# Kernel optimization log

Hardware: AMD Instinct MI355X
Metric: run time of the kernel (lower is better)

Reference implementation:

```python
import jax, jax.numpy as jnp
import numpy as np
from jax import lax

T, B, IN = 50, 1024, 405
H, NMEM, DMEM, R, NWAY = 200, 128, 40, 4, 5
GAMMA = 0.99


def setup_inputs() -> dict:
    key = jax.random.key(0)
    ks = jax.random.split(key, 11)
    s = lambda *sh: 0.05
    return {
        "x": jax.random.normal(ks[0], (T, B, IN), jnp.float32),
        "W_ih": jax.random.normal(ks[1], (4 * H, IN), jnp.float32) * 0.05,
        "W_hh": jax.random.normal(ks[2], (4 * H, H), jnp.float32) * 0.05,
        "b_ih": jax.random.normal(ks[3], (4 * H,), jnp.float32) * 0.05,
        "b_hh": jax.random.normal(ks[4], (4 * H,), jnp.float32) * 0.05,
        "Wk": jax.random.normal(ks[5], (R * DMEM, H), jnp.float32) * 0.05,
        "bk": jax.random.normal(ks[6], (R * DMEM,), jnp.float32) * 0.05,
        "Ws": jax.random.normal(ks[7], (R, H), jnp.float32) * 0.05,
        "bs": jax.random.normal(ks[8], (R,), jnp.float32) * 0.05,
        "Wo": jax.random.normal(ks[9], (NWAY, H + R * DMEM), jnp.float32) * 0.05,
        "bo": jax.random.normal(ks[10], (NWAY,), jnp.float32) * 0.05,
    }


def _ntm_forward(x, W_ih, W_hh, b_ih, b_hh, Wk, bk, Ws, bs, Wo, bo):
    sg = lax.stop_gradient
    batch_idx = jnp.arange(B)

    def step(carry, x_t):
        h, c, M, wr, wu, wlu = carry
        # LSTM cell (torch nn.LSTMCell gate order: i, f, g, o)
        gates = x_t @ W_ih.T + b_ih + h @ W_hh.T + b_hh
        i, f, g, o = jnp.split(gates, 4, axis=-1)
        c = jax.nn.sigmoid(f) * c + jax.nn.sigmoid(i) * jnp.tanh(g)
        h = jax.nn.sigmoid(o) * jnp.tanh(c)
        # zero out least-used memory row (data-level op in torch)
        idx = jnp.argmin(wu, axis=1)
        M = M.at[batch_idx, idx].set(0.0)
        # keys and interpolation gate
        k = jnp.tanh(h @ Wk.T + bk).reshape(B, R, DMEM)
        sigma = jax.nn.sigmoid(jnp.tanh(h @ Ws.T + bs)).reshape(B, R, 1)
        # write weights and memory write
        ww = sigma * wr + (1.0 - sigma) * wlu[:, None, :]  # [B,R,NMEM]
        M = M + jnp.einsum("brm,brd->bmd", ww, k)
        # cosine-similarity read addressing
        nk = jnp.linalg.norm(k, axis=2)   # [B,R]
        nM = jnp.linalg.norm(M, axis=2)   # [B,NMEM]
        K = jnp.einsum("brd,bmd->brm", k, M) / (nk[:, :, None] * nM[:, None, :])
        wr_new = jax.nn.softmax(K, axis=-1)  # softmax over memory slots
        r = jnp.einsum("brm,bmd->brd", wr_new, M).reshape(B, R * DMEM)
        # output head: Linear -> Sigmoid -> Softmax (as in torch source)
        logits = jnp.concatenate([h, r], axis=1) @ Wo.T + bo
        out = jax.nn.softmax(jax.nn.sigmoid(logits), axis=-1)
        # usage update (all detached in torch)
        wr_d = sg(wr_new)
        wu = GAMMA * wu + jnp.sum(wr_d + sg(ww), axis=1)
        kth = -lax.top_k(-wu, R)[0][:, -1]  # k-th smallest usage
        wlu = sg((wu <= kth[:, None]).astype(M.dtype))
        return (h, c, sg(M), wr_d, wu, wlu), out

    carry0 = (
        jnp.zeros((B, H), x.dtype),
        jnp.zeros((B, H), x.dtype),
        jnp.zeros((B, NMEM, DMEM), x.dtype),
        jnp.zeros((B, R, NMEM), x.dtype),
        jnp.zeros((B, NMEM), x.dtype),
        jnp.ones((B, NMEM), x.dtype),
    )
    _, y = lax.scan(step, carry0, x)
    return y  # [T, B, NWAY]


def reference(x, W_ih, W_hh, b_ih, b_hh, Wk, bk, Ws, bs, Wo, bo):
    return _ntm_forward(x, W_ih, W_hh, b_ih, b_hh, Wk, bk, Ws, bs, Wo, bo)
```

## Files before the change

kernel.cpp:

```cpp
#include <hip/hip_runtime.h>
#include <stdint.h>

#define TSTEPS 50
#define BATCH  1024
#define INDIM  405
#define KP     448
#define HDIM   200
#define G4H    800
#define NMEM   128
#define DMEM   40
#define DPAD   44
#define RH     4
#define RD     160
#define NWAY   5
#define GAMMA_ 0.99f
#define NG     2
#define WROWS  928

typedef __attribute__((ext_vector_type(8))) short short8;
typedef __attribute__((ext_vector_type(4))) float f32x4;

__device__ __forceinline__ float sigmoidf_(float x) {
    return 1.f / (1.f + __expf(-x));
}
__device__ __forceinline__ float ftanh(float x) {
    float e = __expf(2.f * x);
    return 1.f - 2.f / (e + 1.f);
}
__device__ __forceinline__ unsigned short f2bf(float f) {
    uint32_t u = __float_as_uint(f);
    uint32_t r = u + 0x7FFFu + ((u >> 16) & 1u);
    return (unsigned short)(r >> 16);
}
__device__ __forceinline__ float bf2f(unsigned short h) {
    return __uint_as_float(((uint32_t)h) << 16);
}
__device__ __forceinline__ float bflo(uint32_t u) { return __uint_as_float(u << 16); }
__device__ __forceinline__ float bfhi(uint32_t u) { return __uint_as_float(u & 0xFFFF0000u); }

__global__ __launch_bounds__(256) void convert_recQ(const float* __restrict__ W_hh,
                                                    const float* __restrict__ Wk,
                                                    uint4* __restrict__ Whh_q4,
                                                    uint2* __restrict__ Wk_q2) {
    int i = blockIdx.x * 256 + threadIdx.x;
    if (i < 50 * 400) {
        int jq = i / 400, p = i % 400;
        int j = jq * 4;
        const float* r0 = W_hh + (2 * p) * HDIM;
        const float* r1 = W_hh + (2 * p + 1) * HDIM;
        uint4 v;
        v.x = (uint32_t)f2bf(r0[j])     | ((uint32_t)f2bf(r0[j + 1]) << 16);
        v.y = (uint32_t)f2bf(r1[j])     | ((uint32_t)f2bf(r1[j + 1]) << 16);
        v.z = (uint32_t)f2bf(r0[j + 2]) | ((uint32_t)f2bf(r0[j + 3]) << 16);
        v.w = (uint32_t)f2bf(r1[j + 2]) | ((uint32_t)f2bf(r1[j + 3]) << 16);
        Whh_q4[i] = v;
    } else if (i < 50 * 400 + 50 * 160) {
        int e = i - 50 * 400;
        int jq = e / 160, col = e % 160;
        int j = jq * 4;
        const float* r = Wk + col * HDIM;
        uint2 v;
        v.x = (uint32_t)f2bf(r[j])     | ((uint32_t)f2bf(r[j + 1]) << 16);
        v.y = (uint32_t)f2bf(r[j + 2]) | ((uint32_t)f2bf(r[j + 3]) << 16);
        Wk_q2[e] = v;
    }
}

__global__ __launch_bounds__(256) void convert_A(const float* __restrict__ x,
                                                 unsigned short* __restrict__ Ahi,
                                                 unsigned short* __restrict__ Alo) {
    int c = blockIdx.x * 256 + threadIdx.x;
    int r = blockIdx.y;
    if (c >= KP) return;
    float v = (c < INDIM) ? x[(size_t)r * INDIM + c] : 0.f;
    unsigned short hi = f2bf(v);
    unsigned short lo = f2bf(v - bf2f(hi));
    size_t o = (size_t)r * KP + c;
    Ahi[o] = hi;
    Alo[o] = lo;
}

__global__ __launch_bounds__(256) void convert_W(const float* __restrict__ W_ih,
                                                 unsigned short* __restrict__ Wpk) {
    int c = blockIdx.x * 256 + threadIdx.x;
    int n = blockIdx.y;
    int sec = blockIdx.z;
    if (c >= KP) return;
    float v = (n < G4H && c < INDIM) ? W_ih[(size_t)n * INDIM + c] : 0.f;
    unsigned short hi = f2bf(v);
    size_t o = (size_t)sec * WROWS * KP + (size_t)n * KP + c;
    Wpk[o] = (sec == 0) ? hi : f2bf(v - bf2f(hi));
}

__global__ __launch_bounds__(256) void gx_gemm_mfma(
        const unsigned short* __restrict__ Ahi,
        const unsigned short* __restrict__ Alo,
        const unsigned short* __restrict__ Wpk,
        const float* __restrict__ b_ih, const float* __restrict__ b_hh,
        float* __restrict__ gx) {
    __shared__ unsigned short Alds[128 * 64];
    __shared__ unsigned short Blds[128 * 64];
    const int tid = threadIdx.x;
    const int wv = tid >> 6, ln = tid & 63;
    const int wr = wv >> 1, wc = wv & 1;
    const int n0 = blockIdx.x * 128;
    const int m0 = blockIdx.y * 128;

    f32x4 acc[4][4];
#pragma unroll
    for (int m = 0; m < 4; ++m)
#pragma unroll
        for (int n = 0; n < 4; ++n) acc[m][n] = (f32x4){0.f, 0.f, 0.f, 0.f};

    int erow[4], ecol[4];
#pragma unroll
    for (int i = 0; i < 4; ++i) {
        int e = (i * 4 + wv) * 512 + ln * 8;
        erow[i] = e >> 6;
        ecol[i] = e & 63;
    }

    const unsigned short* Whi = Wpk;
    const unsigned short* Wlo = Wpk + (size_t)WROWS * KP;

#pragma unroll 1
    for (int s = 0; s < 3; ++s) {
        const unsigned short* Ab = ((s == 2) ? Alo : Ahi) + (size_t)m0 * KP;
        const unsigned short* Bb = ((s == 1) ? Wlo : Whi) + (size_t)n0 * KP;

        short8 ar[4], br[4];
#pragma unroll
        for (int i = 0; i < 4; ++i) {
            ar[i] = *(const short8*)&Ab[(size_t)erow[i] * KP + ecol[i]];
            br[i] = *(const short8*)&Bb[(size_t)erow[i] * KP + ecol[i]];
        }

#pragma unroll 1
        for (int k0 = 0; k0 < KP; k0 += 64) {
            __syncthreads();
#pragma unroll
            for (int i = 0; i < 4; ++i) {
                int e = (i * 4 + wv) * 512 + ln * 8;
                *(short8*)&Alds[e] = ar[i];
                *(short8*)&Blds[e] = br[i];
            }
            __syncthreads();
            if (k0 + 64 < KP) {
#pragma unroll
                for (int i = 0; i < 4; ++i) {
                    ar[i] = *(const short8*)&Ab[(size_t)erow[i] * KP + k0 + 64 + ecol[i]];
                    br[i] = *(const short8*)&Bb[(size_t)erow[i] * KP + k0 + 64 + ecol[i]];
                }
            }
#pragma unroll
            for (int ks = 0; ks < 2; ++ks) {
                short8 af[4], bf[4];
                int kcol = ks * 32 + (ln >> 4) * 8;
#pragma unroll
                for (int m = 0; m < 4; ++m) {
                    int row = wr * 64 + m * 16 + (ln & 15);
                    af[m] = *(const short8*)&Alds[row * 64 + kcol];
                }
#pragma unroll
                for (int n = 0; n < 4; ++n) {
                    int row = wc * 64 + n * 16 + (ln & 15);
                    bf[n] = *(const short8*)&Blds[row * 64 + kcol];
                }
#pragma unroll
                for (int m = 0; m < 4; ++m)
#pragma unroll
                    for (int n = 0; n < 4; ++n)
                        acc[m][n] = __builtin_amdgcn_mfma_f32_16x16x32_bf16(
                            af[m], bf[n], acc[m][n], 0, 0, 0);
            }
        }
    }

#pragma unroll
    for (int n = 0; n < 4; ++n) {
        int col = n0 + wc * 64 + n * 16 + (ln & 15);
        if (col >= G4H) continue;
        float bias = b_ih[col] + b_hh[col];
#pragma unroll
        for (int m = 0; m < 4; ++m) {
#pragma unroll
            for (int j = 0; j < 4; ++j) {
                int row = m0 + wr * 64 + m * 16 + (ln >> 4) * 4 + j;
                gx[(size_t)row * G4H + col] = acc[m][n][j] + bias;
            }
        }
    }
}

__global__ __launch_bounds__(256) void gx_gemm(const float* __restrict__ x,
                                               const float* __restrict__ W_ih,
                                               const float* __restrict__ b_ih,
                                               const float* __restrict__ b_hh,
                                               float* __restrict__ gx) {
    const int BM = 128, BN = 80, BK = 16;
    __shared__ float As[BK][BM];
    __shared__ float Bs[BK][BN];
    int m0 = blockIdx.y * BM;
    int n0 = blockIdx.x * BN;
    int tid = threadIdx.x;
    int tm = tid >> 4, tn = tid & 15;
    float acc[8][5];
#pragma unroll
    for (int i = 0; i < 8; ++i)
#pragma unroll
        for (int j = 0; j < 5; ++j) acc[i][j] = 0.f;

    for (int k0 = 0; k0 < INDIM; k0 += BK) {
        {
            int row = tid >> 1, kk = (tid & 1) * 8;
            const float* ap = x + (size_t)(m0 + row) * INDIM + k0 + kk;
#pragma unroll
            for (int i = 0; i < 8; ++i)
                As[kk + i][row] = (k0 + kk + i < INDIM) ? ap[i] : 0.f;
        }
        if (tid < 160) {
            int col = tid >> 1, kk = (tid & 1) * 8;
            const float* bp = W_ih + (size_t)(n0 + col) * INDIM + k0 + kk;
#pragma unroll
            for (int i = 0; i < 8; ++i)
                Bs[kk + i][col] = (k0 + kk + i < INDIM) ? bp[i] : 0.f;
        }
        __syncthreads();
#pragma unroll
        for (int k = 0; k < BK; ++k) {
            float a[8], b[5];
#pragma unroll
            for (int i = 0; i < 8; ++i) a[i] = As[k][tm * 8 + i];
#pragma unroll
            for (int j = 0; j < 5; ++j) b[j] = Bs[k][tn * 5 + j];
#pragma unroll
            for (int i = 0; i < 8; ++i)
#pragma unroll
                for (int j = 0; j < 5; ++j) acc[i][j] += a[i] * b[j];
        }
        __syncthreads();
    }
#pragma unroll
    for (int j = 0; j < 5; ++j) {
        int n = n0 + tn * 5 + j;
        float bias = b_ih[n] + b_hh[n];
#pragma unroll
        for (int i = 0; i < 8; ++i) {
            int m = m0 + tm * 8 + i;
            gx[(size_t)m * G4H + n] = acc[i][j] + bias;
        }
    }
}

__global__ __launch_bounds__(512, 4) void ntm_scan(
        const float* __restrict__ gx,
        const uint4* __restrict__ Whh_q4,
        const uint2* __restrict__ Wk_q2,
        const float* __restrict__ bk,
        const float* __restrict__ Wsm,
        const float* __restrict__ bs,
        const float* __restrict__ Wo,
        const float* __restrict__ bo,
        float* __restrict__ out) {
    __shared__ float sM[NG][NMEM][DPAD];
    __shared__ float sh[NG][HDIM];
    __shared__ float sgate[NG][G4H];
    __shared__ float spartK[NG][2][RD];
    __shared__ float spartS[NG][RH][4];
    __shared__ float swr[NG][RH][NMEM];
    __shared__ float sww[NG][RH][NMEM];
    __shared__ float sKs[NG][RH][NMEM];
    __shared__ float swu[NG][NMEM];
    __shared__ float swlu[NG][NMEM];
    __shared__ float sk[NG][RH][DMEM];
    __shared__ float sr[NG][RD];
    __shared__ float snk[NG][RH];
    __shared__ float ssig[NG][RH];
    __shared__ float snM[NG][NMEM];
    __shared__ float stmp[NG][NWAY];
    __shared__ int   sidx[NG];

    const int tid = threadIdx.x;
    const int b0  = blockIdx.x * NG;
    const int w   = tid >> 6, l = tid & 63;

    for (int e = tid; e < NG * NMEM * DPAD; e += 512) ((float*)sM)[e] = 0.f;
    for (int e = tid; e < NG * HDIM; e += 512) ((float*)sh)[e] = 0.f;
    for (int e = tid; e < NG * RH * NMEM; e += 512) ((float*)swr)[e] = 0.f;
    for (int e = tid; e < NG * NMEM; e += 512) { ((float*)swu)[e] = 0.f; ((float*)swlu)[e] = 1.f; }

    float c_reg = 0.f;
    float gxr0 = 0.f, gxr1 = 0.f, gxr2 = 0.f, gxr3 = 0.f;
    int pg = 0, pj = 0;
    if (tid < NG * HDIM) {
        pg = tid / HDIM; pj = tid - pg * HDIM;
        const float* gxp = gx + (size_t)(b0 + pg) * G4H + pj;
        gxr0 = gxp[0]; gxr1 = gxp[HDIM]; gxr2 = gxp[2 * HDIM]; gxr3 = gxp[3 * HDIM];
    }
    __syncthreads();

    for (int t = 0; t < TSTEPS; ++t) {
        if (tid < 400) {
            const uint4* wq = Whh_q4 + tid;
            float a00 = 0.f, a01 = 0.f, a10 = 0.f, a11 = 0.f;
#pragma unroll 5
            for (int jq = 0; jq < 50; ++jq) {
                uint4 wv = wq[jq * 400];
                float4 h0 = *(const float4*)&sh[0][jq * 4];
                float4 h1 = *(const float4*)&sh[1][jq * 4];
                float we0 = bflo(wv.x), we1 = bfhi(wv.x);
                float wo0 = bflo(wv.y), wo1 = bfhi(wv.y);
                float we2 = bflo(wv.z), we3 = bfhi(wv.z);
                float wo2 = bflo(wv.w), wo3 = bfhi(wv.w);
                a00 += we0 * h0.x + we1 * h0.y + we2 * h0.z + we3 * h0.w;
                a01 += wo0 * h0.x + wo1 * h0.y + wo2 * h0.z + wo3 * h0.w;
                a10 += we0 * h1.x + we1 * h1.y + we2 * h1.z + we3 * h1.w;
                a11 += wo0 * h1.x + wo1 * h1.y + wo2 * h1.z + wo3 * h1.w;
            }
            sgate[0][2 * tid]     = a00;
            sgate[0][2 * tid + 1] = a01;
            sgate[1][2 * tid]     = a10;
            sgate[1][2 * tid + 1] = a11;
        }
        __syncthreads();

        if (tid < NG * HDIM) {
            float ig = sigmoidf_(sgate[pg][pj] + gxr0);
            float fg = sigmoidf_(sgate[pg][pj + HDIM] + gxr1);
            float gv = ftanh(sgate[pg][pj + 2 * HDIM] + gxr2);
            float og = sigmoidf_(sgate[pg][pj + 3 * HDIM] + gxr3);
            c_reg = fg * c_reg + ig * gv;
            sh[pg][pj] = og * ftanh(c_reg);
            if (t + 1 < TSTEPS) {
                const float* gxp = gx + ((size_t)(t + 1) * BATCH + b0 + pg) * G4H + pj;
                gxr0 = gxp[0]; gxr1 = gxp[HDIM]; gxr2 = gxp[2 * HDIM]; gxr3 = gxp[3 * HDIM];
            }
        }
        __syncthreads();

        if (tid < 320) {
            int col = tid % RD, c = tid / RD;
            const uint2* wq = Wk_q2 + (size_t)(c * 25) * RD + col;
            const int jb = c * 100;
            float a0 = 0.f, a1 = 0.f;
#pragma unroll 5
            for (int q = 0; q < 25; ++q) {
                uint2 wv = wq[q * RD];
                float4 h0 = *(const float4*)&sh[0][jb + q * 4];
                float4 h1 = *(const float4*)&sh[1][jb + q * 4];
                float w0 = bflo(wv.x), w1 = bfhi(wv.x);
                float w2 = bflo(wv.y), w3 = bfhi(wv.y);
                a0 += w0 * h0.x + w1 * h0.y + w2 * h0.z + w3 * h0.w;
                a1 += w0 * h1.x + w1 * h1.y + w2 * h1.z + w3 * h1.w;
            }
            spartK[0][c][col] = a0;
            spartK[1][c][col] = a1;
        } else if (tid < 448) {
            int a = tid - 320; int g = a >> 6, ln = a & 63;
            float v0 = swu[g][ln], v1 = swu[g][ln + 64];
            bool p1 = (v1 < v0);
            float mv = p1 ? v1 : v0;
            int   mi = p1 ? ln + 64 : ln;
#pragma unroll
            for (int off = 32; off; off >>= 1) {
                float ov = __shfl_xor(mv, off);
                int   oi = __shfl_xor(mi, off);
                if (ov < mv || (ov == mv && oi < mi)) { mv = ov; mi = oi; }
            }
            if (ln == 0) sidx[g] = mi;
        } else if (tid < 480) {
            int v = tid - 448; int g = v >> 4, rc = v & 15, r = rc >> 2, cc = rc & 3;
            const float* wrow = Wsm + r * HDIM;
            float a = 0.f;
            for (int j = 50 * cc; j < 50 * cc + 50; ++j) a += sh[g][j] * wrow[j];
            spartS[g][r][cc] = a;
        }
        __syncthreads();

        if (tid < 320) {
            int g = tid / RD, col = tid % RD;
            float s = spartK[g][0][col] + spartK[g][1][col] + bk[col];
            sk[g][col / DMEM][col % DMEM] = ftanh(s);
        } else if (tid < 328) {
            int v = tid - 320; int g = v >> 2, r = v & 3;
            float s = spartS[g][r][0] + spartS[g][r][1]
                    + spartS[g][r][2] + spartS[g][r][3] + bs[r];
            ssig[g][r] = sigmoidf_(ftanh(s));
        }
        __syncthreads();

        {
            int g = tid >> 8, mh = tid & 255, m = mh >> 1, dh = mh & 1;
            float sg0 = ssig[g][0], sg1 = ssig[g][1], sg2 = ssig[g][2], sg3 = ssig[g][3];
            float wl = swlu[g][m];
            float w0 = sg0 * swr[g][0][m] + (1.f - sg0) * wl;
            float w1 = sg1 * swr[g][1][m] + (1.f - sg1) * wl;
            float w2 = sg2 * swr[g][2][m] + (1.f - sg2) * wl;
            float w3 = sg3 * swr[g][3][m] + (1.f - sg3) * wl;
            if (!dh) {
                sww[g][0][m] = w0; sww[g][1][m] = w1;
                sww[g][2][m] = w2; sww[g][3][m] = w3;
            }
            bool zr = (m == sidx[g]);
            int d0 = dh * 20;
#pragma unroll
            for (int q = 0; q < 5; ++q) {
                int d = d0 + q * 4;
                float4 mv = *(const float4*)&sM[g][m][d];
                float4 k0 = *(const float4*)&sk[g][0][d];
                float4 k1 = *(const float4*)&sk[g][1][d];
                float4 k2 = *(const float4*)&sk[g][2][d];
                float4 k3 = *(const float4*)&sk[g][3][d];
                float4 o;
                o.x = (zr ? 0.f : mv.x) + w0 * k0.x + w1 * k1.x + w2 * k2.x + w3 * k3.x;
                o.y = (zr ? 0.f : mv.y) + w0 * k0.y + w1 * k1.y + w2 * k2.y + w3 * k3.y;
                o.z = (zr ? 0.f : mv.z) + w0 * k0.z + w1 * k1.z + w2 * k2.z + w3 * k3.z;
                o.w = (zr ? 0.f : mv.w) + w0 * k0.w + w1 * k1.w + w2 * k2.w + w3 * k3.w;
                *(float4*)&sM[g][m][d] = o;
            }
            if (tid < 8) {
                int g2 = tid >> 2, r2 = tid & 3;
                float a0 = 0.f, a1 = 0.f, a2 = 0.f, a3 = 0.f;
#pragma unroll
                for (int q = 0; q < 10; ++q) {
                    float4 kv = *(const float4*)&sk[g2][r2][q * 4];
                    a0 += kv.x * kv.x; a1 += kv.y * kv.y;
                    a2 += kv.z * kv.z; a3 += kv.w * kv.w;
                }
                snk[g2][r2] = sqrtf((a0 + a1) + (a2 + a3));
            }
        }
        __syncthreads();

#pragma unroll
        for (int q = 0; q < 2; ++q) {
            int e = tid + q * 512;
            int g = e >> 9, rm = e & 511, r = rm >> 7, m = rm & 127;
            float a0 = 0.f, a1 = 0.f, a2 = 0.f, a3 = 0.f;
#pragma unroll
            for (int d4 = 0; d4 < 10; ++d4) {
                float4 kv = *(const float4*)&sk[g][r][d4 * 4];
                float4 mv = *(const float4*)&sM[g][m][d4 * 4];
                a0 += kv.x * mv.x; a1 += kv.y * mv.y;
                a2 += kv.z * mv.z; a3 += kv.w * mv.w;
            }
            sKs[g][r][m] = (a0 + a1) + (a2 + a3);
        }
        if (tid < 256) {
            int g = tid >> 7, m = tid & 127;
            float a0 = 0.f, a1 = 0.f, a2 = 0.f, a3 = 0.f;
#pragma unroll
            for (int d4 = 0; d4 < 10; ++d4) {
                float4 mv = *(const float4*)&sM[g][m][d4 * 4];
                a0 += mv.x * mv.x; a1 += mv.y * mv.y;
                a2 += mv.z * mv.z; a3 += mv.w * mv.w;
            }
            snM[g][m] = sqrtf((a0 + a1) + (a2 + a3));
        }
        __syncthreads();

        {
            int g = w >> 2, r = w & 3, ln = l;
            float ink = snk[g][r];
            float a = sKs[g][r][ln] / (ink * snM[g][ln]);
            float b = sKs[g][r][ln + 64] / (ink * snM[g][ln + 64]);
            float mx = fmaxf(a, b);
#pragma unroll
            for (int off = 32; off; off >>= 1) mx = fmaxf(mx, __shfl_xor(mx, off));
            float ea = __expf(a - mx), eb = __expf(b - mx);
            float s = ea + eb;
#pragma unroll
            for (int off = 32; off; off >>= 1) s += __shfl_xor(s, off);
            float inv = 1.f / s;
            swr[g][r][ln]      = ea * inv;
            swr[g][r][ln + 64] = eb * inv;
        }
        __syncthreads();

        if (tid < 80) {
            int g = tid / 40, rd4 = tid % 40, r = rd4 / 10, d4 = rd4 % 10;
            float a0 = 0.f, a1 = 0.f, a2 = 0.f, a3 = 0.f;
            for (int m = 0; m < NMEM; ++m) {
                float wv = swr[g][r][m];
                float4 mv = *(const float4*)&sM[g][m][d4 * 4];
                a0 += wv * mv.x; a1 += wv * mv.y;
                a2 += wv * mv.z; a3 += wv * mv.w;
            }
            float4 res = {a0, a1, a2, a3};
            *(float4*)&sr[g][r * DMEM + d4 * 4] = res;
        } else if (tid >= 256) {
            int e = tid - 256;
            int g = e >> 7, m = e & 127;
            float wu = GAMMA_ * swu[g][m];
#pragma unroll
            for (int r = 0; r < RH; ++r) wu += swr[g][r][m] + sww[g][r][m];
            swu[g][m] = wu;
        }
        __syncthreads();

        if (tid < 320) {
            int g = tid / RD, v = tid % RD, o = v >> 5, ln = v & 31;
            const float* wrow = Wo + o * (HDIM + RD);
            float acc = 0.f;
            for (int j = ln; j < HDIM; j += 32) acc += sh[g][j] * wrow[j];
            for (int d = ln; d < RD; d += 32) acc += sr[g][d] * wrow[HDIM + d];
#pragma unroll
            for (int off = 16; off; off >>= 1) acc += __shfl_xor(acc, off, 32);
            if (ln == 0) stmp[g][o] = acc + bo[o];
        } else if (tid < 448) {
            int a = tid - 320; int g = a >> 6, ln = a & 63;
            float o0 = swu[g][ln], o1 = swu[g][ln + 64];
            float v0 = o0, v1 = o1, kth = 0.f;
#pragma unroll
            for (int it = 0; it < RH; ++it) {
                bool p1 = (v1 < v0);
                float mv = p1 ? v1 : v0;
                int   mi = p1 ? ln + 64 : ln;
                for (int off = 32; off; off >>= 1) {
                    float ov = __shfl_xor(mv, off);
                    int   oi = __shfl_xor(mi, off);
                    if (ov < mv || (ov == mv && oi < mi)) { mv = ov; mi = oi; }
                }
                kth = mv;
                if (mi == ln) v0 = __builtin_inff();
                else if (mi == ln + 64) v1 = __builtin_inff();
            }
            swlu[g][ln]      = (o0 <= kth) ? 1.f : 0.f;
            swlu[g][ln + 64] = (o1 <= kth) ? 1.f : 0.f;
        }
        __syncthreads();

        if (tid < NG) {
            int g = tid;
            float v[NWAY], mx = -1e30f;
#pragma unroll
            for (int o = 0; o < NWAY; ++o) { v[o] = sigmoidf_(stmp[g][o]); mx = fmaxf(mx, v[o]); }
            float s = 0.f;
#pragma unroll
            for (int o = 0; o < NWAY; ++o) { v[o] = __expf(v[o] - mx); s += v[o]; }
            float inv = 1.f / s;
            float* op = out + ((size_t)t * BATCH + (b0 + g)) * NWAY;
#pragma unroll
            for (int o = 0; o < NWAY; ++o) op[o] = v[o] * inv;
        }
    }
}

extern "C" void kernel_launch(void* const* d_in, const int* in_sizes, int n_in,
                              void* d_out, int out_size, void* d_ws, size_t ws_size,
                              hipStream_t stream) {
    const float* x    = (const float*)d_in[0];
    const float* W_ih = (const float*)d_in[1];
    const float* W_hh = (const float*)d_in[2];
    const float* b_ih = (const float*)d_in[3];
    const float* b_hh = (const float*)d_in[4];
    const float* Wk   = (const float*)d_in[5];
    const float* bk   = (const float*)d_in[6];
    const float* Wsm  = (const float*)d_in[7];
    const float* bs   = (const float*)d_in[8];
    const float* Wo   = (const float*)d_in[9];
    const float* bo   = (const float*)d_in[10];
    float* out = (float*)d_out;

    const size_t gx_elems  = (size_t)TSTEPS * BATCH * G4H;
    const size_t whh_q4_e  = (size_t)50 * 400;
    const size_t wk_q2_e   = (size_t)50 * 160;
    const size_t a_elems   = (size_t)TSTEPS * BATCH * KP;
    const size_t w_elems   = (size_t)2 * WROWS * KP;
    const size_t need_base = gx_elems * 4 + whh_q4_e * 16 + wk_q2_e * 8;
    const size_t need_mfma = need_base + (2 * a_elems + w_elems) * 2;
    if (ws_size < need_base) return;

    float* gxb = (float*)d_ws;
    uint4* Whh_q4 = (uint4*)(gxb + gx_elems);
    uint2* Wk_q2  = (uint2*)(Whh_q4 + whh_q4_e);

    {
        int tot = (int)(whh_q4_e + wk_q2_e);
        convert_recQ<<<dim3((tot + 255) / 256), dim3(256), 0, stream>>>(W_hh, Wk, Whh_q4, Wk_q2);
    }

    if (ws_size >= need_mfma) {
        unsigned short* Ahi = (unsigned short*)(Wk_q2 + wk_q2_e);
        unsigned short* Alo = Ahi + a_elems;
        unsigned short* Wpk = Alo + a_elems;
        convert_A<<<dim3(2, TSTEPS * BATCH), dim3(256), 0, stream>>>(x, Ahi, Alo);
        convert_W<<<dim3(2, WROWS, 2), dim3(256), 0, stream>>>(W_ih, Wpk);
        gx_gemm_mfma<<<dim3(7, (TSTEPS * BATCH) / 128), dim3(256), 0, stream>>>(
            Ahi, Alo, Wpk, b_ih, b_hh, gxb);
    } else {
        gx_gemm<<<dim3(G4H / 80, (TSTEPS * BATCH) / 128), dim3(256), 0, stream>>>(
            x, W_ih, b_ih, b_hh, gxb);
    }

    ntm_scan<<<dim3(BATCH / NG), dim3(512), 0, stream>>>(
        gxb, Whh_q4, Wk_q2, bk, Wsm, bs, Wo, bo, out);
}
```

Measured before the change: 1.539 ms.

## Overlap output head and usage top-k with the next step's LSTM GEMV

Restructures the per-timestep schedule. Two warps now compute the previous step's output head, the argmin and the k-smallest usage mask while the other warps run the W_hh GEMV. The memory update is fused with the cosine dot products and row norms, so one pass writes M and computes K and nM. This removes several __syncthreads barriers per step. In exchange, a few threads do the tail GEMV rows, which lengthens the critical path of that phase, and the update now runs on 256 threads instead of 512.

After: 1.802 ms. 1.17x slower.

```diff
diff --git a/kernel.cpp b/kernel.cpp
--- a/kernel.cpp
+++ b/kernel.cpp
@@ -277,7 +277,6 @@
     __shared__ float snk[NG][RH];
     __shared__ float ssig[NG][RH];
     __shared__ float snM[NG][NMEM];
-    __shared__ float stmp[NG][NWAY];
     __shared__ int   sidx[NG];
 
     const int tid = threadIdx.x;
@@ -299,28 +298,95 @@
     }
     __syncthreads();
 
+    auto head_store = [&](int g, int tt) {
+        float v[NWAY];
+#pragma unroll
+        for (int o = 0; o < NWAY; ++o) {
+            const float* wrow = Wo + o * (HDIM + RD);
+            float acc = 0.f;
+            for (int j = l; j < HDIM; j += 64) acc += sh[g][j] * wrow[j];
+            for (int d = l; d < RD; d += 64) acc += sr[g][d] * wrow[HDIM + d];
+#pragma unroll
+            for (int off = 32; off; off >>= 1) acc += __shfl_xor(acc, off);
+            v[o] = acc + bo[o];
+        }
+        if (l == 0) {
+            float mx = -1e30f;
+#pragma unroll
+            for (int o = 0; o < NWAY; ++o) { v[o] = sigmoidf_(v[o]); mx = fmaxf(mx, v[o]); }
+            float s = 0.f;
+#pragma unroll
+            for (int o = 0; o < NWAY; ++o) { v[o] = __expf(v[o] - mx); s += v[o]; }
+            float inv = 1.f / s;
+            float* op = out + ((size_t)tt * BATCH + (b0 + g)) * NWAY;
+#pragma unroll
+            for (int o = 0; o < NWAY; ++o) op[o] = v[o] * inv;
+        }
+    };
+
+    auto gemv_pair = [&](int p) {
+        const uint4* wq = Whh_q4 + p;
+        float a00 = 0.f, a01 = 0.f, a10 = 0.f, a11 = 0.f;
+#pragma unroll 5
+        for (int jq = 0; jq < 50; ++jq) {
+            uint4 wv = wq[jq * 400];
+            float4 h0 = *(const float4*)&sh[0][jq * 4];
+            float4 h1 = *(const float4*)&sh[1][jq * 4];
+            float we0 = bflo(wv.x), we1 = bfhi(wv.x);
+            float wo0 = bflo(wv.y), wo1 = bfhi(wv.y);
+            float we2 = bflo(wv.z), we3 = bfhi(wv.z);
+            float wo2 = bflo(wv.w), wo3 = bfhi(wv.w);
+            a00 += we0 * h0.x + we1 * h0.y + we2 * h0.z + we3 * h0.w;
+            a01 += wo0 * h0.x + wo1 * h0.y + wo2 * h0.z + wo3 * h0.w;
+            a10 += we0 * h1.x + we1 * h1.y + we2 * h1.z + we3 * h1.w;
+            a11 += wo0 * h1.x + wo1 * h1.y + wo2 * h1.z + wo3 * h1.w;
+        }
+        sgate[0][2 * p]     = a00;
+        sgate[0][2 * p + 1] = a01;
+        sgate[1][2 * p]     = a10;
+        sgate[1][2 * p + 1] = a11;
+    };
+
     for (int t = 0; t < TSTEPS; ++t) {
-        if (tid < 400) {
-            const uint4* wq = Whh_q4 + tid;
-            float a00 = 0.f, a01 = 0.f, a10 = 0.f, a11 = 0.f;
-#pragma unroll 5
-            for (int jq = 0; jq < 50; ++jq) {
-                uint4 wv = wq[jq * 400];
-                float4 h0 = *(const float4*)&sh[0][jq * 4];
-                float4 h1 = *(const float4*)&sh[1][jq * 4];
-                float we0 = bflo(wv.x), we1 = bfhi(wv.x);
-                float wo0 = bflo(wv.y), wo1 = bfhi(wv.y);
-                float we2 = bflo(wv.z), we3 = bfhi(wv.z);
-                float wo2 = bflo(wv.w), wo3 = bfhi(wv.w);
-                a00 += we0 * h0.x + we1 * h0.y + we2 * h0.z + we3 * h0.w;
-                a01 += wo0 * h0.x + wo1 * h0.y + wo2 * h0.z + wo3 * h0.w;
-                a10 += we0 * h1.x + we1 * h1.y + we2 * h1.z + we3 * h1.w;
-                a11 += wo0 * h1.x + wo1 * h1.y + wo2 * h1.z + wo3 * h1.w;
-            }
-            sgate[0][2 * tid]     = a00;
-            sgate[0][2 * tid + 1] = a01;
-            sgate[1][2 * tid]     = a10;
-            sgate[1][2 * tid + 1] = a11;
+        if (tid < 384) {
+            gemv_pair(tid);
+            if (tid < 16) gemv_pair(tid + 384);
+        } else {
+            int g = w - 6;
+            if (t > 0) head_store(g, t - 1);
+            {
+                float v0 = swu[g][l], v1 = swu[g][l + 64];
+                bool p1 = (v1 < v0);
+                float mv = p1 ? v1 : v0;
+                int   mi = p1 ? l + 64 : l;
+#pragma unroll
+                for (int off = 32; off; off >>= 1) {
+                    float ov = __shfl_xor(mv, off);
+                    int   oi = __shfl_xor(mi, off);
+                    if (ov < mv || (ov == mv && oi < mi)) { mv = ov; mi = oi; }
+                }
+                if (l == 0) sidx[g] = mi;
+            }
+            {
+                float o0 = swu[g][l], o1 = swu[g][l + 64];
+                float v0 = o0, v1 = o1, kth = 0.f;
+#pragma unroll
+                for (int it = 0; it < RH; ++it) {
+                    bool p1 = (v1 < v0);
+                    float mv = p1 ? v1 : v0;
+                    int   mi = p1 ? l + 64 : l;
+                    for (int off = 32; off; off >>= 1) {
+                        float ov = __shfl_xor(mv, off);
+                        int   oi = __shfl_xor(mi, off);
+                        if (ov < mv || (ov == mv && oi < mi)) { mv = ov; mi = oi; }
+                    }
+                    kth = mv;
+                    if (mi == l) v0 = __builtin_inff();
+                    else if (mi == l + 64) v1 = __builtin_inff();
+                }
+                swlu[g][l]      = (o0 <= kth) ? 1.f : 0.f;
+                swlu[g][l + 64] = (o1 <= kth) ? 1.f : 0.f;
+            }
         }
         __syncthreads();
 
@@ -355,21 +421,8 @@
             }
             spartK[0][c][col] = a0;
             spartK[1][c][col] = a1;
-        } else if (tid < 448) {
-            int a = tid - 320; int g = a >> 6, ln = a & 63;
-            float v0 = swu[g][ln], v1 = swu[g][ln + 64];
-            bool p1 = (v1 < v0);
-            float mv = p1 ? v1 : v0;
-            int   mi = p1 ? ln + 64 : ln;
-#pragma unroll
-            for (int off = 32; off; off >>= 1) {
-                float ov = __shfl_xor(mv, off);
-                int   oi = __shfl_xor(mi, off);
-                if (ov < mv || (ov == mv && oi < mi)) { mv = ov; mi = oi; }
-            }
-            if (ln == 0) sidx[g] = mi;
-        } else if (tid < 480) {
-            int v = tid - 448; int g = v >> 4, rc = v & 15, r = rc >> 2, cc = rc & 3;
+        } else if (tid < 352) {
+            int v = tid - 320; int g = v >> 4, rc = v & 15, r = rc >> 2, cc = rc & 3;
             const float* wrow = Wsm + r * HDIM;
             float a = 0.f;
             for (int j = 50 * cc; j < 50 * cc + 50; ++j) a += sh[g][j] * wrow[j];
@@ -389,23 +442,21 @@
         }
         __syncthreads();
 
-        {
-            int g = tid >> 8, mh = tid & 255, m = mh >> 1, dh = mh & 1;
+        if (tid < 256) {
+            int g = tid >> 7, m = tid & 127;
             float sg0 = ssig[g][0], sg1 = ssig[g][1], sg2 = ssig[g][2], sg3 = ssig[g][3];
             float wl = swlu[g][m];
             float w0 = sg0 * swr[g][0][m] + (1.f - sg0) * wl;
             float w1 = sg1 * swr[g][1][m] + (1.f - sg1) * wl;
             float w2 = sg2 * swr[g][2][m] + (1.f - sg2) * wl;
             float w3 = sg3 * swr[g][3][m] + (1.f - sg3) * wl;
-            if (!dh) {
-                sww[g][0][m] = w0; sww[g][1][m] = w1;
-                sww[g][2][m] = w2; sww[g][3][m] = w3;
-            }
+            sww[g][0][m] = w0; sww[g][1][m] = w1;
+            sww[g][2][m] = w2; sww[g][3][m] = w3;
             bool zr = (m == sidx[g]);
-            int d0 = dh * 20;
-#pragma unroll
-            for (int q = 0; q < 5; ++q) {
-                int d = d0 + q * 4;
+            float d0 = 0.f, d1 = 0.f, d2 = 0.f, d3 = 0.f, nn = 0.f;
+#pragma unroll
+            for (int q = 0; q < 10; ++q) {
+                int d = q * 4;
                 float4 mv = *(const float4*)&sM[g][m][d];
                 float4 k0 = *(const float4*)&sk[g][0][d];
                 float4 k1 = *(const float4*)&sk[g][1][d];
@@ -417,45 +468,25 @@
                 o.z = (zr ? 0.f : mv.z) + w0 * k0.z + w1 * k1.z + w2 * k2.z + w3 * k3.z;
                 o.w = (zr ? 0.f : mv.w) + w0 * k0.w + w1 * k1.w + w2 * k2.w + w3 * k3.w;
                 *(float4*)&sM[g][m][d] = o;
-            }
-            if (tid < 8) {
-                int g2 = tid >> 2, r2 = tid & 3;
-                float a0 = 0.f, a1 = 0.f, a2 = 0.f, a3 = 0.f;
-#pragma unroll
-                for (int q = 0; q < 10; ++q) {
-                    float4 kv = *(const float4*)&sk[g2][r2][q * 4];
-                    a0 += kv.x * kv.x; a1 += kv.y * kv.y;
-                    a2 += kv.z * kv.z; a3 += kv.w * kv.w;
-                }
-                snk[g2][r2] = sqrtf((a0 + a1) + (a2 + a3));
-            }
-        }
-        __syncthreads();
-
-#pragma unroll
-        for (int q = 0; q < 2; ++q) {
-            int e = tid + q * 512;
-            int g = e >> 9, rm = e & 511, r = rm >> 7, m = rm & 127;
+                d0 += k0.x * o.x + k0.y * o.y + k0.z * o.z + k0.w * o.w;
+                d1 += k1.x * o.x + k1.y * o.y + k1.z * o.z + k1.w * o.w;
+                d2 += k2.x * o.x + k2.y * o.y + k2.z * o.z + k2.w * o.w;
+                d3 += k3.x * o.x + k3.y * o.y + k3.z * o.z + k3.w * o.w;
+                nn += o.x * o.x + o.y * o.y + o.z * o.z + o.w * o.w;
+            }
+            sKs[g][0][m] = d0; sKs[g][1][m] = d1;
+            sKs[g][2][m] = d2; sKs[g][3][m] = d3;
+            snM[g][m] = sqrtf(nn);
+        } else if (tid < 264) {
+            int v = tid - 256; int g2 = v >> 2, r2 = v & 3;
             float a0 = 0.f, a1 = 0.f, a2 = 0.f, a3 = 0.f;
 #pragma unroll
-            for (int d4 = 0; d4 < 10; ++d4) {
-                float4 kv = *(const float4*)&sk[g][r][d4 * 4];
-                float4 mv = *(const float4*)&sM[g][m][d4 * 4];
-                a0 += kv.x * mv.x; a1 += kv.y * mv.y;
-                a2 += kv.z * mv.z; a3 += kv.w * mv.w;
-            }
-            sKs[g][r][m] = (a0 + a1) + (a2 + a3);
-        }
-        if (tid < 256) {
-            int g = tid >> 7, m = tid & 127;
-            float a0 = 0.f, a1 = 0.f, a2 = 0.f, a3 = 0.f;
-#pragma unroll
-            for (int d4 = 0; d4 < 10; ++d4) {
-                float4 mv = *(const float4*)&sM[g][m][d4 * 4];
-                a0 += mv.x * mv.x; a1 += mv.y * mv.y;
-                a2 += mv.z * mv.z; a3 += mv.w * mv.w;
-            }
-            snM[g][m] = sqrtf((a0 + a1) + (a2 + a3));
+            for (int q = 0; q < 10; ++q) {
+                float4 kv = *(const float4*)&sk[g2][r2][q * 4];
+                a0 += kv.x * kv.x; a1 += kv.y * kv.y;
+                a2 += kv.z * kv.z; a3 += kv.w * kv.w;
+            }
+            snk[g2][r2] = sqrtf((a0 + a1) + (a2 + a3));
         }
         __syncthreads();
 
@@ -497,53 +528,9 @@
             swu[g][m] = wu;
         }
         __syncthreads();
-
-        if (tid < 320) {
-            int g = tid / RD, v = tid % RD, o = v >> 5, ln = v & 31;
-            const float* wrow = Wo + o * (HDIM + RD);
-            float acc = 0.f;
-            for (int j = ln; j < HDIM; j += 32) acc += sh[g][j] * wrow[j];
-            for (int d = ln; d < RD; d += 32) acc += sr[g][d] * wrow[HDIM + d];
-#pragma unroll
-            for (int off = 16; off; off >>= 1) acc += __shfl_xor(acc, off, 32);
-            if (ln == 0) stmp[g][o] = acc + bo[o];
-        } else if (tid < 448) {
-            int a = tid - 320; int g = a >> 6, ln = a & 63;
-            float o0 = swu[g][ln], o1 = swu[g][ln + 64];
-            float v0 = o0, v1 = o1, kth = 0.f;
-#pragma unroll
-            for (int it = 0; it < RH; ++it) {
-                bool p1 = (v1 < v0);
-                float mv = p1 ? v1 : v0;
-                int   mi = p1 ? ln + 64 : ln;
-                for (int off = 32; off; off >>= 1) {
-                    float ov = __shfl_xor(mv, off);
-                    int   oi = __shfl_xor(mi, off);
-                    if (ov < mv || (ov == mv && oi < mi)) { mv = ov; mi = oi; }
-                }
-                kth = mv;
-                if (mi == ln) v0 = __builtin_inff();
-                else if (mi == ln + 64) v1 = __builtin_inff();
-            }
-            swlu[g][ln]      = (o0 <= kth) ? 1.f : 0.f;
-            swlu[g][ln + 64] = (o1 <= kth) ? 1.f : 0.f;
-        }
-        __syncthreads();
-
-        if (tid < NG) {
-            int g = tid;
-            float v[NWAY], mx = -1e30f;
-#pragma unroll
-            for (int o = 0; o < NWAY; ++o) { v[o] = sigmoidf_(stmp[g][o]); mx = fmaxf(mx, v[o]); }
-            float s = 0.f;
-#pragma unroll
-            for (int o = 0; o < NWAY; ++o) { v[o] = __expf(v[o] - mx); s += v[o]; }
-            float inv = 1.f / s;
-            float* op = out + ((size_t)t * BATCH + (b0 + g)) * NWAY;
-#pragma unroll
-            for (int o = 0; o < NWAY; ++o) op[o] = v[o] * inv;
-        }
-    }
+    }
+
+    if (w >= 6) head_store(w - 6, TSTEPS - 1);
 }
 
 extern "C" void kernel_launch(void* const* d_in, const int* in_sizes, int n_in,
```
